# Optimization experiments

Hardware: AMD Instinct MI355X
Metric: run time of the kernel (lower is better)

Reference implementation:

```python
import jax, jax.numpy as jnp
import numpy as np

B, M, D = 16384, 9, 512
DELTA = 0.5


def setup_inputs() -> dict:
    key = jax.random.key(0)
    k0, k1, k2, k3, k4 = jax.random.split(key, 5)
    s = 1.0 / np.sqrt(D).astype(np.float32)
    return {
        "x": jax.random.normal(k0, (B, M, D), jnp.float32),
        "Wi": jax.random.normal(k1, (M, D, D), jnp.float32) * s,
        "bi": jax.random.normal(k2, (M, D), jnp.float32) * s,
        "We": jax.random.normal(k3, (M, D, D), jnp.float32) * s,
        "be": jax.random.normal(k4, (M, D), jnp.float32) * s,
    }


def reference(x, Wi, bi, We, be):
    # ---- IntraRM: per-branch Linear+Sigmoid, L1-norm gating ----
    # batched per-branch GEMM: [B,M,D] x [M,D,D] -> [B,M,D]
    f = jax.nn.sigmoid(jnp.einsum('bmd,mde->bme', x, Wi) + bi)
    alphas = jnp.sum(jnp.abs(f), axis=-1)          # [B, M]  (L1 norm)
    feats = alphas[:, :, None] * x                  # [B, M, D]
    # ---- InterRM: per-branch Linear+ReLU, cdist affinity, tanh-masked matmul ----
    g = jax.nn.relu(jnp.einsum('bmd,mde->bme', feats, We) + be)  # [B, M, D]
    sq = jnp.sum(g * g, axis=-1)                    # [B, M]
    d2 = sq[:, :, None] + sq[:, None, :] - 2.0 * jnp.einsum('bmd,bnd->bmn', g, g)
    d2 = jnp.maximum(d2, 0.0)
    # safe sqrt (torch.cdist, p=2); diagonal d2==0 handled without NaN grads
    dist = jnp.where(d2 > 0, jnp.sqrt(jnp.where(d2 > 0, d2, 1.0)), 0.0)
    mask = 1.0 - jnp.eye(M, dtype=g.dtype)          # zero self-affinity
    affin = jnp.tanh(dist) * mask                   # [B, M, M]
    g_hat = jnp.einsum('bmn,bnd->bmd', affin, g)    # aggregate across branches
    out = DELTA * g + (1.0 - DELTA) * g_hat
    return out, alphas
```

## Files before the change

### kernel.cpp

```cpp
#include <hip/hip_runtime.h>
#include <hip/hip_bf16.h>
#include <hip/hip_fp16.h>

#define BATCH 16384
#define NM 9
#define ND 512
#define BM 64
#define NKT 16
#define NTHREADS 512
#define WMAT ((size_t)ND * ND)

typedef __bf16 bf16x8 __attribute__((ext_vector_type(8)));
typedef float  f32x4  __attribute__((ext_vector_type(4)));

__global__ __launch_bounds__(256)
void prep_weights(const float* __restrict__ Wi, const float* __restrict__ We,
                  __hip_bfloat16* __restrict__ WiT, __hip_bfloat16* __restrict__ WeT) {
  const int z  = blockIdx.y;
  const int kt = blockIdx.x;
  const float* src;
  __hip_bfloat16* dst;
  if (z < NM) { src = Wi + (size_t)z * WMAT;        dst = WiT + (size_t)z * WMAT; }
  else        { src = We + (size_t)(z - NM) * WMAT; dst = WeT + (size_t)(z - NM) * WMAT; }
  const int wave = threadIdx.x >> 6;
  const int lane = threadIdx.x & 63;
  const int k0   = kt * 32 + (lane >> 4) * 8;
  #pragma unroll
  for (int g = wave; g < 32; g += 4) {
    const int col = g * 16 + (lane & 15);
    bf16x8 v;
    #pragma unroll
    for (int j = 0; j < 8; ++j)
      v[j] = (__bf16)src[(size_t)(k0 + j) * ND + col];
    *(bf16x8*)(dst + (size_t)(kt * 32 + g) * 512 + lane * 8) = v;
  }
}

__global__ __launch_bounds__(NTHREADS, 4)
void gemm_kernel(const float* __restrict__ x,
                 const __hip_bfloat16* __restrict__ WiT,
                 const __hip_bfloat16* __restrict__ WeT,
                 const float* __restrict__ bi,
                 const float* __restrict__ be,
                 float* __restrict__ out) {
  __shared__ union {
    __hip_bfloat16 xs[BM][ND + 8];
    __half         gs[BM][ND + 8];
  } sh;
  __shared__ float alphaW[8][BM];
  __shared__ float alphaV[BM];

  const int tid  = threadIdx.x;
  const int wave = tid >> 6;
  const int lane = tid & 63;
  const int l15  = lane & 15;
  const int l4   = lane >> 4;

  const int bid = blockIdx.x;
  const int q   = bid >> 3;
  const int m   = q >> 5;
  const int bx  = (bid & 7) + ((q & 31) << 3);
  const int b0  = bx * BM;
  const int wn0 = wave * 64;

  float* alpha_out = out + (size_t)BATCH * NM * ND;

  #pragma unroll
  for (int it = 0; it < (BM * ND / 4) / NTHREADS; ++it) {
    int idx = it * NTHREADS + tid;
    int r   = idx >> 7;
    int c4  = (idx & 127) * 4;
    float4 v = *(const float4*)(x + (size_t)(b0 + r) * (NM * ND) + m * ND + c4);
    union { ushort4 u; __hip_bfloat16 h[4]; } p;
    p.h[0] = __float2bfloat16(v.x);
    p.h[1] = __float2bfloat16(v.y);
    p.h[2] = __float2bfloat16(v.z);
    p.h[3] = __float2bfloat16(v.w);
    *(ushort4*)&sh.xs[r][c4] = p.u;
  }
  __syncthreads();

  for (int pass = 0; pass < 2; ++pass) {
    const __hip_bfloat16* bp =
        (pass ? WeT : WiT) + (size_t)m * WMAT + (size_t)wave * 4 * 512 + lane * 8;

    f32x4 acc[4][4];
    #pragma unroll
    for (int a = 0; a < 4; ++a)
      #pragma unroll
      for (int c = 0; c < 4; ++c) acc[a][c] = (f32x4){0.f, 0.f, 0.f, 0.f};

    bf16x8 breg[2][4];
    #pragma unroll
    for (int nt = 0; nt < 4; ++nt) breg[0][nt] = *(const bf16x8*)(bp + nt * 512);
    #pragma unroll
    for (int nt = 0; nt < 4; ++nt) breg[1][nt] = *(const bf16x8*)(bp + 16384 + nt * 512);

    #pragma unroll
    for (int kt = 0; kt < NKT; ++kt) {
      bf16x8 bnx[4];
      if (kt + 2 < NKT) {
        const __hip_bfloat16* bp2 = bp + (size_t)(kt + 2) * 16384;
        #pragma unroll
        for (int nt = 0; nt < 4; ++nt) bnx[nt] = *(const bf16x8*)(bp2 + nt * 512);
      }
      bf16x8 af[4];
      const int kbase = kt * 32 + l4 * 8;
      #pragma unroll
      for (int mt = 0; mt < 4; ++mt)
        af[mt] = *(const bf16x8*)&sh.xs[mt * 16 + l15][kbase];
      #pragma unroll
      for (int mt = 0; mt < 4; ++mt)
        #pragma unroll
        for (int nt = 0; nt < 4; ++nt)
          acc[mt][nt] = __builtin_amdgcn_mfma_f32_16x16x32_bf16(af[mt], breg[kt & 1][nt], acc[mt][nt], 0, 0, 0);
      if (kt + 2 < NKT) {
        #pragma unroll
        for (int nt = 0; nt < 4; ++nt) breg[kt & 1][nt] = bnx[nt];
      }
    }

    if (pass == 0) {
      float biv[4];
      #pragma unroll
      for (int nt = 0; nt < 4; ++nt) biv[nt] = bi[m * ND + wn0 + nt * 16 + l15];
      #pragma unroll
      for (int mt = 0; mt < 4; ++mt)
        #pragma unroll
        for (int r = 0; r < 4; ++r) {
          float s = 0.f;
          #pragma unroll
          for (int nt = 0; nt < 4; ++nt) {
            float t = acc[mt][nt][r] + biv[nt];
            s += 1.f / (1.f + __expf(-t));
          }
          s += __shfl_xor(s, 1, 16);
          s += __shfl_xor(s, 2, 16);
          s += __shfl_xor(s, 4, 16);
          s += __shfl_xor(s, 8, 16);
          if (l15 == 0) alphaW[wave][mt * 16 + l4 * 4 + r] = s;
        }
      __syncthreads();
      if (tid < BM) {
        float a = 0.f;
        #pragma unroll
        for (int w = 0; w < 8; ++w) a += alphaW[w][tid];
        alphaV[tid] = a;
        alpha_out[(size_t)(b0 + tid) * NM + m] = a;
      }
      __syncthreads();
    } else {
      float bev[4];
      #pragma unroll
      for (int nt = 0; nt < 4; ++nt) bev[nt] = be[m * ND + wn0 + nt * 16 + l15];
      __syncthreads();
      #pragma unroll
      for (int mt = 0; mt < 4; ++mt)
        #pragma unroll
        for (int r = 0; r < 4; ++r) {
          const int row = mt * 16 + l4 * 4 + r;
          const float al = alphaV[row];
          #pragma unroll
          for (int nt = 0; nt < 4; ++nt) {
            float t = fmaxf(al * acc[mt][nt][r] + bev[nt], 0.f);
            sh.gs[row][wn0 + nt * 16 + l15] = __float2half(t);
          }
        }
      __syncthreads();
      #pragma unroll
      for (int i = 0; i < 8; ++i) {
        const int row = wave + i * 8;
        __half* gd = (__half*)((char*)out + (size_t)(b0 + row) * (NM * ND * 4)) + m * ND;
        *(uint4*)(gd + lane * 8) = *(const uint4*)&sh.gs[row][lane * 8];
      }
    }
  }
}

__global__ __launch_bounds__(256)
void inter_kernel(float* __restrict__ out) {
  __shared__ float gs[NM][ND + 8];
  __shared__ float Gr[45];
  __shared__ float aff[NM][NM];
  const int b = blockIdx.x;
  const int tid = threadIdx.x;
  const __half* gsrc = (const __half*)((const char*)out + (size_t)b * (NM * ND * 4));

  for (int i = tid; i < NM * ND / 4; i += 256) {
    union { ushort4 u; __half h[4]; } p;
    p.u = *(const ushort4*)((const ushort*)gsrc + (size_t)i * 4);
    const int m = i >> 7;
    const int e = (i & 127) * 4;
    #pragma unroll
    for (int j = 0; j < 4; ++j) gs[m][e + j] = __half2float(p.h[j]);
  }
  __syncthreads();

  const int wave = tid >> 6, lane = tid & 63;
  for (int pr = wave; pr < 45; pr += 4) {
    int a = 0, qq = pr;
    while (qq >= NM - a) { qq -= NM - a; ++a; }
    const int bb = a + qq;
    float s = 0.f;
    #pragma unroll
    for (int j = 0; j < 8; ++j) s += gs[a][lane + 64 * j] * gs[bb][lane + 64 * j];
    #pragma unroll
    for (int off = 1; off < 64; off <<= 1) s += __shfl_xor(s, off, 64);
    if (lane == 0) Gr[pr] = s;
  }
  __syncthreads();

  if (tid < NM * NM) {
    const int mm = tid / NM, nn = tid % NM;
    float v = 0.f;
    if (mm != nn) {
      const int a = mm < nn ? mm : nn;
      const int c = mm < nn ? nn : mm;
      auto tri = [](int t) { return t * NM - (t * (t - 1)) / 2; };
      float d2 = Gr[tri(mm)] + Gr[tri(nn)] - 2.f * Gr[tri(a) + (c - a)];
      d2 = fmaxf(d2, 0.f);
      v = tanhf(sqrtf(d2));
    }
    aff[tid / NM][tid % NM] = v;
  }
  __syncthreads();

  float* od = out + (size_t)b * (NM * ND);
  for (int i = tid; i < NM * ND / 4; i += 256) {
    const int mm = i >> 7;
    const int e4 = (i & 127) * 4;
    float4 r;
    #pragma unroll
    for (int j = 0; j < 4; ++j) {
      const int e = e4 + j;
      float acc = 0.f;
      #pragma unroll
      for (int n = 0; n < NM; ++n) acc += aff[mm][n] * gs[n][e];
      ((float*)&r)[j] = 0.5f * (gs[mm][e] + acc);
    }
    *(float4*)(od + (size_t)mm * ND + e4) = r;
  }
}

extern "C" void kernel_launch(void* const* d_in, const int* in_sizes, int n_in,
                              void* d_out, int out_size, void* d_ws, size_t ws_size,
                              hipStream_t stream) {
  const float* x  = (const float*)d_in[0];
  const float* Wi = (const float*)d_in[1];
  const float* bi = (const float*)d_in[2];
  const float* We = (const float*)d_in[3];
  const float* be = (const float*)d_in[4];
  float* out = (float*)d_out;

  __hip_bfloat16* WiT = (__hip_bfloat16*)d_ws;
  __hip_bfloat16* WeT = WiT + (size_t)NM * ND * ND;

  prep_weights<<<dim3(NKT, 2 * NM), 256, 0, stream>>>(Wi, We, WiT, WeT);
  gemm_kernel<<<BATCH / BM * NM, NTHREADS, 0, stream>>>(x, WiT, WeT, bi, be, out);
  inter_kernel<<<BATCH, 256, 0, stream>>>(out);
}
```

Before: 410.6 us.

## Fuse Wi and We GEMM passes into one K-loop sharing A fragments

Runs both branch GEMMs (x·Wi and x·We) in a single K loop, using the algebraic fact that (alpha*x)·We = alpha*(x·We). Each LDS fragment of x is then reused for both weight matrices and the second K loop is removed. The cost is twice the accumulator registers (32 f32x4 tiles), which is why launch bounds drop from 4 to 2 waves per SIMD, lowering occupancy. Weight prefetch changes from two tiles ahead to one tile ahead.

```diff
diff --git a/kernel.cpp b/kernel.cpp
--- a/kernel.cpp
+++ b/kernel.cpp
@@ -36,7 +36,7 @@
   }
 }
 
-__global__ __launch_bounds__(NTHREADS, 4)
+__global__ __launch_bounds__(NTHREADS, 2)
 void gemm_kernel(const float* __restrict__ x,
                  const __hip_bfloat16* __restrict__ WiT,
                  const __hip_bfloat16* __restrict__ WeT,
@@ -65,6 +65,15 @@
 
   float* alpha_out = out + (size_t)BATCH * NM * ND;
 
+  const __hip_bfloat16* bpi = WiT + (size_t)m * WMAT + (size_t)wave * 4 * 512 + lane * 8;
+  const __hip_bfloat16* bpe = WeT + (size_t)m * WMAT + (size_t)wave * 4 * 512 + lane * 8;
+
+  bf16x8 breg[2][2][4];
+  #pragma unroll
+  for (int nt = 0; nt < 4; ++nt) breg[0][0][nt] = *(const bf16x8*)(bpi + nt * 512);
+  #pragma unroll
+  for (int nt = 0; nt < 4; ++nt) breg[0][1][nt] = *(const bf16x8*)(bpe + nt * 512);
+
   #pragma unroll
   for (int it = 0; it < (BM * ND / 4) / NTHREADS; ++it) {
     int idx = it * NTHREADS + tid;
@@ -80,99 +89,95 @@
   }
   __syncthreads();
 
-  for (int pass = 0; pass < 2; ++pass) {
-    const __hip_bfloat16* bp =
-        (pass ? WeT : WiT) + (size_t)m * WMAT + (size_t)wave * 4 * 512 + lane * 8;
-
-    f32x4 acc[4][4];
+  f32x4 acc[2][4][4];
+  #pragma unroll
+  for (int pp = 0; pp < 2; ++pp)
     #pragma unroll
     for (int a = 0; a < 4; ++a)
       #pragma unroll
-      for (int c = 0; c < 4; ++c) acc[a][c] = (f32x4){0.f, 0.f, 0.f, 0.f};
-
-    bf16x8 breg[2][4];
-    #pragma unroll
-    for (int nt = 0; nt < 4; ++nt) breg[0][nt] = *(const bf16x8*)(bp + nt * 512);
-    #pragma unroll
-    for (int nt = 0; nt < 4; ++nt) breg[1][nt] = *(const bf16x8*)(bp + 16384 + nt * 512);
-
-    #pragma unroll
-    for (int kt = 0; kt < NKT; ++kt) {
-      bf16x8 bnx[4];
-      if (kt + 2 < NKT) {
-        const __hip_bfloat16* bp2 = bp + (size_t)(kt + 2) * 16384;
+      for (int c = 0; c < 4; ++c) acc[pp][a][c] = (f32x4){0.f, 0.f, 0.f, 0.f};
+
+  #pragma unroll
+  for (int kt = 0; kt < NKT; ++kt) {
+    if (kt + 1 < NKT) {
+      const size_t off = (size_t)(kt + 1) * 16384;
+      #pragma unroll
+      for (int nt = 0; nt < 4; ++nt)
+        breg[(kt + 1) & 1][0][nt] = *(const bf16x8*)(bpi + off + nt * 512);
+      #pragma unroll
+      for (int nt = 0; nt < 4; ++nt)
+        breg[(kt + 1) & 1][1][nt] = *(const bf16x8*)(bpe + off + nt * 512);
+    }
+    bf16x8 af[4];
+    const int kbase = kt * 32 + l4 * 8;
+    #pragma unroll
+    for (int mt = 0; mt < 4; ++mt)
+      af[mt] = *(const bf16x8*)&sh.xs[mt * 16 + l15][kbase];
+    #pragma unroll
+    for (int mt = 0; mt < 4; ++mt)
+      #pragma unroll
+      for (int nt = 0; nt < 4; ++nt)
+        acc[0][mt][nt] = __builtin_amdgcn_mfma_f32_16x16x32_bf16(af[mt], breg[kt & 1][0][nt], acc[0][mt][nt], 0, 0, 0);
+    #pragma unroll
+    for (int mt = 0; mt < 4; ++mt)
+      #pragma unroll
+      for (int nt = 0; nt < 4; ++nt)
+        acc[1][mt][nt] = __builtin_amdgcn_mfma_f32_16x16x32_bf16(af[mt], breg[kt & 1][1][nt], acc[1][mt][nt], 0, 0, 0);
+  }
+
+  {
+    float biv[4];
+    #pragma unroll
+    for (int nt = 0; nt < 4; ++nt) biv[nt] = bi[m * ND + wn0 + nt * 16 + l15];
+    #pragma unroll
+    for (int mt = 0; mt < 4; ++mt)
+      #pragma unroll
+      for (int r = 0; r < 4; ++r) {
+        float s = 0.f;
         #pragma unroll
-        for (int nt = 0; nt < 4; ++nt) bnx[nt] = *(const bf16x8*)(bp2 + nt * 512);
+        for (int nt = 0; nt < 4; ++nt) {
+          float t = acc[0][mt][nt][r] + biv[nt];
+          s += 1.f / (1.f + __expf(-t));
+        }
+        s += __shfl_xor(s, 1, 16);
+        s += __shfl_xor(s, 2, 16);
+        s += __shfl_xor(s, 4, 16);
+        s += __shfl_xor(s, 8, 16);
+        if (l15 == 0) alphaW[wave][mt * 16 + l4 * 4 + r] = s;
       }
-      bf16x8 af[4];
-      const int kbase = kt * 32 + l4 * 8;
-      #pragma unroll
-      for (int mt = 0; mt < 4; ++mt)
-        af[mt] = *(const bf16x8*)&sh.xs[mt * 16 + l15][kbase];
-      #pragma unroll
-      for (int mt = 0; mt < 4; ++mt)
+    __syncthreads();
+    if (tid < BM) {
+      float a = 0.f;
+      #pragma unroll
+      for (int w = 0; w < 8; ++w) a += alphaW[w][tid];
+      alphaV[tid] = a;
+      alpha_out[(size_t)(b0 + tid) * NM + m] = a;
+    }
+    __syncthreads();
+  }
+
+  {
+    float bev[4];
+    #pragma unroll
+    for (int nt = 0; nt < 4; ++nt) bev[nt] = be[m * ND + wn0 + nt * 16 + l15];
+    #pragma unroll
+    for (int mt = 0; mt < 4; ++mt)
+      #pragma unroll
+      for (int r = 0; r < 4; ++r) {
+        const int row = mt * 16 + l4 * 4 + r;
+        const float al = alphaV[row];
         #pragma unroll
-        for (int nt = 0; nt < 4; ++nt)
-          acc[mt][nt] = __builtin_amdgcn_mfma_f32_16x16x32_bf16(af[mt], breg[kt & 1][nt], acc[mt][nt], 0, 0, 0);
-      if (kt + 2 < NKT) {
-        #pragma unroll
-        for (int nt = 0; nt < 4; ++nt) breg[kt & 1][nt] = bnx[nt];
+        for (int nt = 0; nt < 4; ++nt) {
+          float t = fmaxf(al * acc[1][mt][nt][r] + bev[nt], 0.f);
+          sh.gs[row][wn0 + nt * 16 + l15] = __float2half(t);
+        }
       }
-    }
-
-    if (pass == 0) {
-      float biv[4];
-      #pragma unroll
-      for (int nt = 0; nt < 4; ++nt) biv[nt] = bi[m * ND + wn0 + nt * 16 + l15];
-      #pragma unroll
-      for (int mt = 0; mt < 4; ++mt)
-        #pragma unroll
-        for (int r = 0; r < 4; ++r) {
-          float s = 0.f;
-          #pragma unroll
-          for (int nt = 0; nt < 4; ++nt) {
-            float t = acc[mt][nt][r] + biv[nt];
-            s += 1.f / (1.f + __expf(-t));
-          }
-          s += __shfl_xor(s, 1, 16);
-          s += __shfl_xor(s, 2, 16);
-          s += __shfl_xor(s, 4, 16);
-          s += __shfl_xor(s, 8, 16);
-          if (l15 == 0) alphaW[wave][mt * 16 + l4 * 4 + r] = s;
-        }
-      __syncthreads();
-      if (tid < BM) {
-        float a = 0.f;
-        #pragma unroll
-        for (int w = 0; w < 8; ++w) a += alphaW[w][tid];
-        alphaV[tid] = a;
-        alpha_out[(size_t)(b0 + tid) * NM + m] = a;
-      }
-      __syncthreads();
-    } else {
-      float bev[4];
-      #pragma unroll
-      for (int nt = 0; nt < 4; ++nt) bev[nt] = be[m * ND + wn0 + nt * 16 + l15];
-      __syncthreads();
-      #pragma unroll
-      for (int mt = 0; mt < 4; ++mt)
-        #pragma unroll
-        for (int r = 0; r < 4; ++r) {
-          const int row = mt * 16 + l4 * 4 + r;
-          const float al = alphaV[row];
-          #pragma unroll
-          for (int nt = 0; nt < 4; ++nt) {
-            float t = fmaxf(al * acc[mt][nt][r] + bev[nt], 0.f);
-            sh.gs[row][wn0 + nt * 16 + l15] = __float2half(t);
-          }
-        }
-      __syncthreads();
-      #pragma unroll
-      for (int i = 0; i < 8; ++i) {
-        const int row = wave + i * 8;
-        __half* gd = (__half*)((char*)out + (size_t)(b0 + row) * (NM * ND * 4)) + m * ND;
-        *(uint4*)(gd + lane * 8) = *(const uint4*)&sh.gs[row][lane * 8];
-      }
+    __syncthreads();
+    #pragma unroll
+    for (int i = 0; i < 8; ++i) {
+      const int row = wave + i * 8;
+      __half* gd = (__half*)((char*)out + (size_t)(b0 + row) * (NM * ND * 4)) + m * ND;
+      *(uint4*)(gd + lane * 8) = *(const uint4*)&sh.gs[row][lane * 8];
     }
   }
 }
```

After: 459.2 us. 1.12x slower.
